# Kernel optimization log

Measured on AMD Instinct MI355X. Metric: run time of the kernel, lower is better.

## Reference

```python
import jax, jax.numpy as jnp
import numpy as np

BATCH, K, N = 16384, 512, 1024  # codewords, message_length, code_length


def setup_inputs() -> dict:
    key = jax.random.key(0)
    kx, km = jax.random.split(key)
    # binary message bits as float32 (as the torch module casts with .float())
    x = jnp.round(jax.random.uniform(kx, (BATCH, K), dtype=jnp.float32))
    # binary polar generator matrix [K, N]
    matrix = jnp.round(jax.random.uniform(km, (K, N), dtype=jnp.float32))
    return {"x": x, "matrix": matrix}


def reference(x, matrix):
    # GF(2) encoding: (x @ G) mod 2, returned as integer codeword bits
    codeword = jnp.remainder(x @ matrix, 2.0)
    return codeword.astype(jnp.int32)
```

## Files before the change

### kernel.cpp

```cpp
#include <hip/hip_runtime.h>
#include <stdint.h>

#define BATCH 16384
#define KDIM  512
#define NDIM  1024
#define NW    16
#define ROWS_PER_BLOCK 32
#define PHASE_ROWS 8
#define NPHASE (ROWS_PER_BLOCK / PHASE_ROWS)

__global__ __launch_bounds__(256) void pack_g_kernel(const float* __restrict__ G,
                                                     uint32_t* __restrict__ Gt) {
    int t = blockIdx.x * 256 + threadIdx.x;
    int n = t & (NDIM - 1);
    int m = t >> 10;
    int kbase = 256 * (m >> 3) + 128 * ((m >> 2) & 1) + (m & 3);
    uint32_t w = 0;
#pragma unroll
    for (int c = 0; c < 32; ++c) {
        w |= (uint32_t)(G[(size_t)(kbase + 4 * c) * NDIM + n] > 0.5f) << c;
    }
    Gt[t] = w;
}

__global__ __launch_bounds__(1024, 8)
void gf2_fused_kernel(const float* __restrict__ x,
                      const uint32_t* __restrict__ Gt,
                      int* __restrict__ out) {
    const int tid = threadIdx.x;
    const int w   = tid >> 6;
    const int l   = tid & 63;
    const int q   = w >> 1;
    const int h   = w & 1;
    const int row0 = blockIdx.x * ROWS_PER_BLOCK;

    uint32_t g[NW];
#pragma unroll
    for (int m = 0; m < NW; ++m) g[m] = Gt[m * NDIM + tid];

    __shared__ __align__(16) uint32_t xw[2][PHASE_ROWS][NW];

    const float4* xf = reinterpret_cast<const float4*>(x);
    float4 f = xf[(size_t)row0 * (KDIM / 4) + tid];

    for (int p = 0; p < NPHASE; ++p) {
        uint64_t b0 = __ballot(f.x > 0.5f);
        uint64_t b1 = __ballot(f.y > 0.5f);
        uint64_t b2 = __ballot(f.z > 0.5f);
        uint64_t b3 = __ballot(f.w > 0.5f);

        if (p + 1 < NPHASE)
            f = xf[(size_t)(row0 + (p + 1) * PHASE_ROWS) * (KDIM / 4) + tid];

        if (l == 0) {
            uint32_t* dst = &xw[p & 1][q][h * 8];
            dst[0] = (uint32_t)b0;  dst[4] = (uint32_t)(b0 >> 32);
            dst[1] = (uint32_t)b1;  dst[5] = (uint32_t)(b1 >> 32);
            dst[2] = (uint32_t)b2;  dst[6] = (uint32_t)(b2 >> 32);
            dst[3] = (uint32_t)b3;  dst[7] = (uint32_t)(b3 >> 32);
        }
        __syncthreads();

        size_t obase = (size_t)(row0 + p * PHASE_ROWS) * NDIM + tid;
#pragma unroll
        for (int r = 0; r < PHASE_ROWS; ++r) {
            const uint4* x4 = reinterpret_cast<const uint4*>(&xw[p & 1][r][0]);
            uint4 a = x4[0];
            uint32_t t = (a.x & g[0])  ^ (a.y & g[1])  ^ (a.z & g[2])  ^ (a.w & g[3]);
            a = x4[1];
            t ^= (a.x & g[4])  ^ (a.y & g[5])  ^ (a.z & g[6])  ^ (a.w & g[7]);
            a = x4[2];
            t ^= (a.x & g[8])  ^ (a.y & g[9])  ^ (a.z & g[10]) ^ (a.w & g[11]);
            a = x4[3];
            t ^= (a.x & g[12]) ^ (a.y & g[13]) ^ (a.z & g[14]) ^ (a.w & g[15]);
            out[obase + (size_t)r * NDIM] = (int)(__popc(t) & 1u);
        }
    }
}

extern "C" void kernel_launch(void* const* d_in, const int* in_sizes, int n_in,
                              void* d_out, int out_size, void* d_ws, size_t ws_size,
                              hipStream_t stream) {
    const float* x = (const float*)d_in[0];
    const float* G = (const float*)d_in[1];
    int* out = (int*)d_out;

    uint32_t* Gt = (uint32_t*)d_ws;

    pack_g_kernel<<<(NW * NDIM) / 256, 256, 0, stream>>>(G, Gt);
    gf2_fused_kernel<<<BATCH / ROWS_PER_BLOCK, 1024, 0, stream>>>(x, Gt, out);
}
```

Measured before the change: 27.27 us.

## Compute two output columns per thread with half-size blocks

Each thread now holds two columns of the packed generator matrix, loaded as uint2, and produces two codeword bits per row. The output is written as int2. Block size drops from 1024 to 512 threads with 16 rows per block, and the launch-bounds occupancy hint changes accordingly. The aim is to reuse each shared-memory read of the packed message bits across two columns and to widen the global stores. In exchange, register pressure doubles for the generator words and each block does fewer rows per phase.

Result: no change. 27.43 us (+0.6%).

```diff
diff --git a/kernel.cpp b/kernel.cpp
--- a/kernel.cpp
+++ b/kernel.cpp
@@ -5,8 +5,9 @@
 #define KDIM  512
 #define NDIM  1024
 #define NW    16
-#define ROWS_PER_BLOCK 32
-#define PHASE_ROWS 8
+#define THREADS 512
+#define ROWS_PER_BLOCK 16
+#define PHASE_ROWS 4
 #define NPHASE (ROWS_PER_BLOCK / PHASE_ROWS)
 
 __global__ __launch_bounds__(256) void pack_g_kernel(const float* __restrict__ G,
@@ -23,7 +24,7 @@
     Gt[t] = w;
 }
 
-__global__ __launch_bounds__(1024, 8)
+__global__ __launch_bounds__(THREADS, 6)
 void gf2_fused_kernel(const float* __restrict__ x,
                       const uint32_t* __restrict__ Gt,
                       int* __restrict__ out) {
@@ -34,9 +35,13 @@
     const int h   = w & 1;
     const int row0 = blockIdx.x * ROWS_PER_BLOCK;
 
-    uint32_t g[NW];
+    uint32_t g0[NW], g1[NW];
 #pragma unroll
-    for (int m = 0; m < NW; ++m) g[m] = Gt[m * NDIM + tid];
+    for (int m = 0; m < NW; ++m) {
+        uint2 gg = reinterpret_cast<const uint2*>(Gt + m * NDIM)[tid];
+        g0[m] = gg.x;
+        g1[m] = gg.y;
+    }
 
     __shared__ __align__(16) uint32_t xw[2][PHASE_ROWS][NW];
 
@@ -61,19 +66,23 @@
         }
         __syncthreads();
 
-        size_t obase = (size_t)(row0 + p * PHASE_ROWS) * NDIM + tid;
+        size_t obase = (size_t)(row0 + p * PHASE_ROWS) * NDIM + 2 * (size_t)tid;
 #pragma unroll
         for (int r = 0; r < PHASE_ROWS; ++r) {
             const uint4* x4 = reinterpret_cast<const uint4*>(&xw[p & 1][r][0]);
-            uint4 a = x4[0];
-            uint32_t t = (a.x & g[0])  ^ (a.y & g[1])  ^ (a.z & g[2])  ^ (a.w & g[3]);
-            a = x4[1];
-            t ^= (a.x & g[4])  ^ (a.y & g[5])  ^ (a.z & g[6])  ^ (a.w & g[7]);
-            a = x4[2];
-            t ^= (a.x & g[8])  ^ (a.y & g[9])  ^ (a.z & g[10]) ^ (a.w & g[11]);
-            a = x4[3];
-            t ^= (a.x & g[12]) ^ (a.y & g[13]) ^ (a.z & g[14]) ^ (a.w & g[15]);
-            out[obase + (size_t)r * NDIM] = (int)(__popc(t) & 1u);
+            uint4 a0 = x4[0], a1 = x4[1], a2 = x4[2], a3 = x4[3];
+            uint32_t t0 = (a0.x & g0[0])  ^ (a0.y & g0[1])  ^ (a0.z & g0[2])  ^ (a0.w & g0[3])
+                        ^ (a1.x & g0[4])  ^ (a1.y & g0[5])  ^ (a1.z & g0[6])  ^ (a1.w & g0[7])
+                        ^ (a2.x & g0[8])  ^ (a2.y & g0[9])  ^ (a2.z & g0[10]) ^ (a2.w & g0[11])
+                        ^ (a3.x & g0[12]) ^ (a3.y & g0[13]) ^ (a3.z & g0[14]) ^ (a3.w & g0[15]);
+            uint32_t t1 = (a0.x & g1[0])  ^ (a0.y & g1[1])  ^ (a0.z & g1[2])  ^ (a0.w & g1[3])
+                        ^ (a1.x & g1[4])  ^ (a1.y & g1[5])  ^ (a1.z & g1[6])  ^ (a1.w & g1[7])
+                        ^ (a2.x & g1[8])  ^ (a2.y & g1[9])  ^ (a2.z & g1[10]) ^ (a2.w & g1[11])
+                        ^ (a3.x & g1[12]) ^ (a3.y & g1[13]) ^ (a3.z & g1[14]) ^ (a3.w & g1[15]);
+            int2 o;
+            o.x = (int)(__popc(t0) & 1u);
+            o.y = (int)(__popc(t1) & 1u);
+            *reinterpret_cast<int2*>(out + obase + (size_t)r * NDIM) = o;
         }
     }
 }
@@ -88,5 +97,5 @@
     uint32_t* Gt = (uint32_t*)d_ws;
 
     pack_g_kernel<<<(NW * NDIM) / 256, 256, 0, stream>>>(G, Gt);
-    gf2_fused_kernel<<<BATCH / ROWS_PER_BLOCK, 1024, 0, stream>>>(x, Gt, out);
+    gf2_fused_kernel<<<BATCH / ROWS_PER_BLOCK, THREADS, 0, stream>>>(x, Gt, out);
 }
```

## Pre-pack x into bit words in separate kernel; two columns per thread in GEMM

Applied to the files above, without the earlier changes.

Moves the x bit-packing out of the fused kernel (ballot plus shared memory plus barriers) into a combined pack kernel that also packs G with a contiguous k-bit layout via a shared-memory reduction. The GEMM kernel then reads packed x rows directly from global memory, with no barriers, and each thread computes two output columns with a vectorized int2 store. This removes per-block synchronisation and the in-kernel ballot packing, at the cost of an extra round trip of packed x through global memory and doubled register use for G.

After: 30.23 us. +10.8%, slower.

```diff
diff --git a/kernel.cpp b/kernel.cpp
--- a/kernel.cpp
+++ b/kernel.cpp
@@ -5,76 +5,84 @@
 #define KDIM  512
 #define NDIM  1024
 #define NW    16
-#define ROWS_PER_BLOCK 32
-#define PHASE_ROWS 8
-#define NPHASE (ROWS_PER_BLOCK / PHASE_ROWS)
 
-__global__ __launch_bounds__(256) void pack_g_kernel(const float* __restrict__ G,
-                                                     uint32_t* __restrict__ Gt) {
-    int t = blockIdx.x * 256 + threadIdx.x;
-    int n = t & (NDIM - 1);
-    int m = t >> 10;
-    int kbase = 256 * (m >> 3) + 128 * ((m >> 2) & 1) + (m & 3);
-    uint32_t w = 0;
+typedef int i32x2 __attribute__((ext_vector_type(2)));
+
+__global__ __launch_bounds__(256) void pack_kernel(const float* __restrict__ x,
+                                                   const float* __restrict__ G,
+                                                   uint32_t* __restrict__ xp,
+                                                   uint32_t* __restrict__ Gt) {
+    const int bid = blockIdx.x;
+    if (bid < 1024) {
+        int t = bid * 256 + threadIdx.x;
+        const float4* xf = reinterpret_cast<const float4*>(x) + (size_t)t * 8;
+        uint32_t w = 0;
 #pragma unroll
-    for (int c = 0; c < 32; ++c) {
-        w |= (uint32_t)(G[(size_t)(kbase + 4 * c) * NDIM + n] > 0.5f) << c;
+        for (int u = 0; u < 8; ++u) {
+            float4 f = xf[u];
+            w |= (uint32_t)(f.x > 0.5f) << (4 * u + 0);
+            w |= (uint32_t)(f.y > 0.5f) << (4 * u + 1);
+            w |= (uint32_t)(f.z > 0.5f) << (4 * u + 2);
+            w |= (uint32_t)(f.w > 0.5f) << (4 * u + 3);
+        }
+        xp[t] = w;
+    } else {
+        __shared__ uint32_t nib[8][32];
+        const int b  = bid - 1024;
+        const int m  = b >> 5;
+        const int n0 = (b & 31) << 5;
+        const int p  = threadIdx.x >> 5;
+        const int nn = threadIdx.x & 31;
+        uint32_t w = 0;
+#pragma unroll
+        for (int j = 0; j < 4; ++j) {
+            int c = 4 * p + j;
+            w |= (uint32_t)(G[(size_t)(m * 32 + c) * NDIM + n0 + nn] > 0.5f) << c;
+        }
+        nib[p][nn] = w;
+        __syncthreads();
+        if (threadIdx.x < 32) {
+            uint32_t r = nib[0][threadIdx.x] | nib[1][threadIdx.x]
+                       | nib[2][threadIdx.x] | nib[3][threadIdx.x]
+                       | nib[4][threadIdx.x] | nib[5][threadIdx.x]
+                       | nib[6][threadIdx.x] | nib[7][threadIdx.x];
+            Gt[m * NDIM + n0 + threadIdx.x] = r;
+        }
     }
-    Gt[t] = w;
 }
 
-__global__ __launch_bounds__(1024, 8)
-void gf2_fused_kernel(const float* __restrict__ x,
-                      const uint32_t* __restrict__ Gt,
-                      int* __restrict__ out) {
+#define BROWS 32
+__global__ __launch_bounds__(512, 4)
+void gf2_gemm_kernel(const uint32_t* __restrict__ xp,
+                     const uint32_t* __restrict__ Gt,
+                     int* __restrict__ out) {
     const int tid = threadIdx.x;
-    const int w   = tid >> 6;
-    const int l   = tid & 63;
-    const int q   = w >> 1;
-    const int h   = w & 1;
-    const int row0 = blockIdx.x * ROWS_PER_BLOCK;
 
-    uint32_t g[NW];
+    uint32_t g0[NW], g1[NW];
 #pragma unroll
-    for (int m = 0; m < NW; ++m) g[m] = Gt[m * NDIM + tid];
+    for (int i = 0; i < NW; ++i) {
+        uint2 gg = reinterpret_cast<const uint2*>(Gt + i * NDIM)[tid];
+        g0[i] = gg.x;
+        g1[i] = gg.y;
+    }
 
-    __shared__ __align__(16) uint32_t xw[2][PHASE_ROWS][NW];
-
-    const float4* xf = reinterpret_cast<const float4*>(x);
-    float4 f = xf[(size_t)row0 * (KDIM / 4) + tid];
-
-    for (int p = 0; p < NPHASE; ++p) {
-        uint64_t b0 = __ballot(f.x > 0.5f);
-        uint64_t b1 = __ballot(f.y > 0.5f);
-        uint64_t b2 = __ballot(f.z > 0.5f);
-        uint64_t b3 = __ballot(f.w > 0.5f);
-
-        if (p + 1 < NPHASE)
-            f = xf[(size_t)(row0 + (p + 1) * PHASE_ROWS) * (KDIM / 4) + tid];
-
-        if (l == 0) {
-            uint32_t* dst = &xw[p & 1][q][h * 8];
-            dst[0] = (uint32_t)b0;  dst[4] = (uint32_t)(b0 >> 32);
-            dst[1] = (uint32_t)b1;  dst[5] = (uint32_t)(b1 >> 32);
-            dst[2] = (uint32_t)b2;  dst[6] = (uint32_t)(b2 >> 32);
-            dst[3] = (uint32_t)b3;  dst[7] = (uint32_t)(b3 >> 32);
-        }
-        __syncthreads();
-
-        size_t obase = (size_t)(row0 + p * PHASE_ROWS) * NDIM + tid;
-#pragma unroll
-        for (int r = 0; r < PHASE_ROWS; ++r) {
-            const uint4* x4 = reinterpret_cast<const uint4*>(&xw[p & 1][r][0]);
-            uint4 a = x4[0];
-            uint32_t t = (a.x & g[0])  ^ (a.y & g[1])  ^ (a.z & g[2])  ^ (a.w & g[3]);
-            a = x4[1];
-            t ^= (a.x & g[4])  ^ (a.y & g[5])  ^ (a.z & g[6])  ^ (a.w & g[7]);
-            a = x4[2];
-            t ^= (a.x & g[8])  ^ (a.y & g[9])  ^ (a.z & g[10]) ^ (a.w & g[11]);
-            a = x4[3];
-            t ^= (a.x & g[12]) ^ (a.y & g[13]) ^ (a.z & g[14]) ^ (a.w & g[15]);
-            out[obase + (size_t)r * NDIM] = (int)(__popc(t) & 1u);
-        }
+    const int row0 = blockIdx.x * BROWS;
+#pragma unroll 4
+    for (int r = 0; r < BROWS; ++r) {
+        const uint4* xr = reinterpret_cast<const uint4*>(xp + (size_t)(row0 + r) * NW);
+        uint4 xa = xr[0], xb = xr[1], xc = xr[2], xd = xr[3];
+        uint32_t t0 = (xa.x & g0[0])  ^ (xa.y & g0[1])  ^ (xa.z & g0[2])  ^ (xa.w & g0[3])
+                    ^ (xb.x & g0[4])  ^ (xb.y & g0[5])  ^ (xb.z & g0[6])  ^ (xb.w & g0[7])
+                    ^ (xc.x & g0[8])  ^ (xc.y & g0[9])  ^ (xc.z & g0[10]) ^ (xc.w & g0[11])
+                    ^ (xd.x & g0[12]) ^ (xd.y & g0[13]) ^ (xd.z & g0[14]) ^ (xd.w & g0[15]);
+        uint32_t t1 = (xa.x & g1[0])  ^ (xa.y & g1[1])  ^ (xa.z & g1[2])  ^ (xa.w & g1[3])
+                    ^ (xb.x & g1[4])  ^ (xb.y & g1[5])  ^ (xb.z & g1[6])  ^ (xb.w & g1[7])
+                    ^ (xc.x & g1[8])  ^ (xc.y & g1[9])  ^ (xc.z & g1[10]) ^ (xc.w & g1[11])
+                    ^ (xd.x & g1[12]) ^ (xd.y & g1[13]) ^ (xd.z & g1[14]) ^ (xd.w & g1[15]);
+        i32x2 o;
+        o.x = (int)(__popc(t0) & 1u);
+        o.y = (int)(__popc(t1) & 1u);
+        *reinterpret_cast<i32x2*>(out + (size_t)(row0 + r) * NDIM + 2 * (size_t)tid) = o;
     }
 }
 
@@ -85,8 +93,9 @@
     const float* G = (const float*)d_in[1];
     int* out = (int*)d_out;
 
-    uint32_t* Gt = (uint32_t*)d_ws;
+    uint32_t* xp = (uint32_t*)d_ws;
+    uint32_t* Gt = (uint32_t*)((char*)d_ws + (size_t)BATCH * NW * 4);
 
-    pack_g_kernel<<<(NW * NDIM) / 256, 256, 0, stream>>>(G, Gt);
-    gf2_fused_kernel<<<BATCH / ROWS_PER_BLOCK, 1024, 0, stream>>>(x, Gt, out);
+    pack_kernel<<<1024 + 512, 256, 0, stream>>>(x, G, xp, Gt);
+    gf2_gemm_kernel<<<BATCH / BROWS, 512, 0, stream>>>(xp, Gt, out);
 }
```
